# Kernel optimization log

Measured on AMD Instinct MI355X. Metric: run time of the kernel, lower is better.

## Reference

```python
import jax, jax.numpy as jnp
import numpy as np
import math
from jax import lax

B, C, T = 32, 256, 1024
KS = 64          # key_size
KERN = 3         # conv kernel size
PAD = 2          # (KERN-1)*dilation, chomped -> causal left pad
SQRT_KS = math.sqrt(KS)


def setup_inputs() -> dict:
    key = jax.random.key(0)
    ks = jax.random.split(key, 14)
    s = 0.01
    return {
        "x":  jax.random.normal(ks[0], (B, C, T), jnp.float32),
        # attention linears (stored [in, out])
        "wq": jax.random.normal(ks[1], (C, KS), jnp.float32) * s,
        "bq": jnp.zeros((KS,), jnp.float32),
        "wk": jax.random.normal(ks[2], (C, KS), jnp.float32) * s,
        "bk": jnp.zeros((KS,), jnp.float32),
        "wv": jax.random.normal(ks[3], (C, C), jnp.float32) * s,
        "bv": jnp.zeros((C,), jnp.float32),
        # weight-normed conv 1: v [out,in,k], g [out], b [out]
        "v1": jax.random.normal(ks[4], (C, C, KERN), jnp.float32) * s,
        "g1": jnp.ones((C,), jnp.float32),
        "b1": jnp.zeros((C,), jnp.float32),
        # weight-normed conv 2
        "v2": jax.random.normal(ks[5], (C, C, KERN), jnp.float32) * s,
        "g2": jnp.ones((C,), jnp.float32),
        "b2": jnp.zeros((C,), jnp.float32),
    }


def _wn_conv_relu(h, v, g, b):
    # weight_norm (dim=0): W = g * v / ||v||, norm over (in, k) per out channel
    norm = jnp.sqrt(jnp.sum(v * v, axis=(1, 2), keepdims=True))
    W = (g[:, None, None] / norm) * v
    # left-pad PAD == Conv1d(padding=PAD) + Chomp1d(PAD)  (causal conv)
    y = lax.conv_general_dilated(h, W, window_strides=(1,), padding=[(PAD, 0)],
                                 dimension_numbers=("NCH", "OIH", "NCH"))
    return jax.nn.relu(y + b[None, :, None])


def reference(x, wq, bq, wk, bk, wv, bv, v1, g1, b1, v2, g2, b2):
    t = x.shape[2]
    xt = jnp.swapaxes(x, 1, 2)                      # [B, T, C]
    q = xt @ wq + bq                                # [B, T, KS]
    k = xt @ wk + bk                                # [B, T, KS]
    v = xt @ wv + bv                                # [B, T, C]
    scores = jnp.einsum("bqd,bkd->bqk", q, k)       # [B, Tq, Tk]
    # torch mask[j][i] = 1 if i > j -> masked where key index > query index
    idx = jnp.arange(t)
    mask = idx[None, :] > idx[:, None]              # [Tq, Tk]
    scores = jnp.where(mask[None], -jnp.inf, scores)
    # NOTE: source applies softmax over dim=1 (the QUERY axis) — faithful quirk
    attn = jax.nn.softmax(scores / SQRT_KS, axis=1)  # [B, Tq, Tk]
    out_attn = jnp.einsum("bqk,bkc->bqc", attn, v)  # [B, T, C]
    out_attn = jnp.swapaxes(out_attn, 1, 2)         # [B, C, T]
    # conv stack (dropout=0 / eval)
    out = _wn_conv_relu(out_attn, v1, g1, b1)
    out = _wn_conv_relu(out, v2, g2, b2)
    # en_res branch: per-timestep scaling of x by softmaxed attention mass
    weight_x = jax.nn.softmax(jnp.sum(attn, axis=2), axis=1)  # [B, T]
    en_res_x = weight_x[:, None, :] * x                       # [B, C, T]
    # downsample is None (n_inputs == n_outputs)
    return jax.nn.relu(out + x + en_res_x)
```

## Files before the change

kernel.cpp:

```cpp
#include <hip/hip_runtime.h>
#include <math.h>

#define BB 32
#define CC 256
#define TT 1024

typedef __attribute__((ext_vector_type(4))) float f4;
typedef __attribute__((ext_vector_type(4))) float f32x4;
typedef __attribute__((ext_vector_type(16))) float f32x16;
typedef __attribute__((ext_vector_type(8))) short s8;
typedef __attribute__((ext_vector_type(4))) short s4v;

__device__ inline short f2bf(float f) {
    unsigned u = __builtin_bit_cast(unsigned, f);
    u = (u + 0x7FFFu + ((u >> 16) & 1u)) >> 16;
    return (short)u;
}

static const size_t OFF_QBF  = 0;
static const size_t OFF_KBF  = 4194304;
static const size_t OFF_VT   = 8388608;
static const size_t OFF_OA   = 25165824;
static const size_t OFF_C1   = 58720256;
static const size_t OFF_CRZ  = 75497472;
static const size_t OFF_RS   = 75628544;
static const size_t OFF_WX   = 75759616;
static const size_t OFF_W1   = 75890688;
static const size_t OFF_W2   = 76283904;
static const size_t OFF_WQKV = 76677120;

__global__ __launch_bounds__(256)
void wn_kernel(const float* __restrict__ v1, const float* __restrict__ g1,
               const float* __restrict__ v2, const float* __restrict__ g2,
               short* __restrict__ w1bf, short* __restrict__ w2bf) {
    __shared__ float red[4];
    int which = blockIdx.x >> 8, o = blockIdx.x & 255;
    const float* v = which ? v2 : v1;
    const float* g = which ? g2 : g1;
    short* wt = which ? w2bf : w1bf;
    const float* row = v + (size_t)o * 768;
    int tid = threadIdx.x, lane = tid & 63, wv_ = tid >> 6;
    float r0 = row[tid], r1 = row[tid + 256], r2 = row[tid + 512];
    float s = r0 * r0 + r1 * r1 + r2 * r2;
    for (int d = 1; d < 64; d <<= 1) s += __shfl_xor(s, d, 64);
    if (lane == 0) red[wv_] = s;
    __syncthreads();
    float scale = g[o] * rsqrtf(red[0] + red[1] + red[2] + red[3]);
    for (int j = 0; j < 3; ++j)
        wt[((size_t)(j * 256 + o)) * 256 + tid] = f2bf(scale * row[tid * 3 + j]);
}

__global__ __launch_bounds__(256)
void pack_kernel(const float* __restrict__ wq, const float* __restrict__ wk,
                 const float* __restrict__ wv, short* __restrict__ wqkvbf) {
    int n = blockIdx.x * 4 + (threadIdx.x >> 6);
    int c0 = (threadIdx.x & 63) * 4;
    for (int p = 0; p < 4; ++p) {
        int c = c0 + p;
        float w;
        if (n < 64)       w = wq[c * 64 + n];
        else if (n < 128) w = wk[c * 64 + n - 64];
        else              w = wv[c * 256 + n - 128];
        wqkvbf[(size_t)n * 256 + c] = f2bf(w);
    }
}

__global__ void transpose_kernel(const float* __restrict__ x, short* __restrict__ xt) {
    __shared__ float Tt[64 * 68];
    int tid = threadIdx.x;
    int c0 = blockIdx.x * 64, t0 = blockIdx.y * 64, b = blockIdx.z;
    for (int it = 0; it < 4; ++it) {
        int idx = tid + 256 * it;
        int cr = idx >> 4, tc = idx & 15;
        f4 v = *reinterpret_cast<const f4*>(&x[((size_t)b * CC + c0 + cr) * TT + t0 + tc * 4]);
        *reinterpret_cast<f4*>(&Tt[cr * 68 + tc * 4]) = v;
    }
    __syncthreads();
    for (int it = 0; it < 2; ++it) {
        int idx = tid + 256 * it;
        int tl = idx >> 3, seg = idx & 7;
        s8 o;
        for (int p = 0; p < 8; ++p) o[p] = f2bf(Tt[(seg * 8 + p) * 68 + tl]);
        *reinterpret_cast<s8*>(&xt[((size_t)b * TT + t0 + tl) * CC + c0 + seg * 8]) = o;
    }
}

__global__ __launch_bounds__(256, 3)
void qkv_kernel(const short* __restrict__ xt, const short* __restrict__ wqkv,
                const float* __restrict__ bq, const float* __restrict__ bk,
                const float* __restrict__ bv,
                short* __restrict__ qbf, short* __restrict__ kbf, short* __restrict__ vt) {
    __shared__ short SL[128 * 72 + 64 * 72];
    short* Asm = SL;
    short* Bsm = SL + 128 * 72;
    int tid = threadIdx.x, wv_ = tid >> 6, lane = tid & 63;
    int n15 = lane & 15, quad = lane >> 4;
    int bid = blockIdx.x;
    int r = bid & 7, n = (bid >> 3) % 6, qd = bid / 48;
    int bt = qd * 8 + r;
    int b = bt >> 3, t0 = (bt & 7) * 128;
    int n0 = n * 64;

    f32x4 acc[2][4];
    for (int i = 0; i < 2; ++i) for (int j = 0; j < 4; ++j)
        for (int p = 0; p < 4; ++p) acc[i][j][p] = 0.f;

    for (int kc = 0; kc < 4; ++kc) {
        int c0 = kc * 64;
        __syncthreads();
        for (int it = 0; it < 4; ++it) {
            int idx = tid + 256 * it;
            int row = idx >> 3, seg = idx & 7;
            *reinterpret_cast<s8*>(&Asm[row * 72 + seg * 8]) =
                *reinterpret_cast<const s8*>(&xt[((size_t)b * TT + t0 + row) * CC + c0 + seg * 8]);
        }
        for (int it = 0; it < 2; ++it) {
            int idx = tid + 256 * it;
            int row = idx >> 3, seg = idx & 7;
            *reinterpret_cast<s8*>(&Bsm[row * 72 + seg * 8]) =
                *reinterpret_cast<const s8*>(&wqkv[(size_t)(n0 + row) * 256 + c0 + seg * 8]);
        }
        __syncthreads();
        for (int ks = 0; ks < 2; ++ks)
            for (int mt2 = 0; mt2 < 2; ++mt2) {
                s8 a = *reinterpret_cast<const s8*>(&Asm[(wv_ * 32 + mt2 * 16 + n15) * 72 + quad * 8 + ks * 32]);
                for (int nt = 0; nt < 4; ++nt) {
                    s8 bb = *reinterpret_cast<const s8*>(&Bsm[(nt * 16 + n15) * 72 + quad * 8 + ks * 32]);
                    acc[mt2][nt] = __builtin_amdgcn_mfma_f32_16x16x32_bf16(a, bb, acc[mt2][nt], 0, 0, 0);
                }
            }
    }
    if (n0 < 128) {
        short* outp = (n0 == 0) ? qbf : kbf;
        const float* bias = (n0 == 0) ? bq : bk;
        for (int mt2 = 0; mt2 < 2; ++mt2)
            for (int nt = 0; nt < 4; ++nt) {
                int n_ = nt * 16 + n15;
                float bvl = bias[n_];
                for (int reg = 0; reg < 4; ++reg) {
                    int t = t0 + wv_ * 32 + mt2 * 16 + quad * 4 + reg;
                    outp[((size_t)b * TT + t) * 64 + n_] = f2bf(acc[mt2][nt][reg] + bvl);
                }
            }
    } else {
        int cbase = n0 - 128;
        __syncthreads();
        short* Tw = SL + wv_ * 3072;
        for (int mt2 = 0; mt2 < 2; ++mt2)
            for (int nt = 0; nt < 4; ++nt) {
                int n_ = nt * 16 + n15;
                float bvl = bv[cbase + n_];
                for (int reg = 0; reg < 4; ++reg)
                    Tw[n_ * 48 + mt2 * 16 + quad * 4 + reg] = f2bf(acc[mt2][nt][reg] + bvl);
            }
        for (int p = 0; p < 4; ++p) {
            int n_ = (lane >> 2) + 16 * p;
            int seg = lane & 3;
            s8 vv = *reinterpret_cast<const s8*>(&Tw[n_ * 48 + seg * 8]);
            *reinterpret_cast<s8*>(&vt[((size_t)b * CC + cbase + n_) * TT + t0 + wv_ * 32 + seg * 8]) = vv;
        }
    }
}

__global__ __launch_bounds__(512, 2)
void colz_kernel(const short* __restrict__ qbf, const short* __restrict__ kbf,
                 float* __restrict__ colrz) {
    __shared__ short Qs[4][64 * 72];
    __shared__ short Ks[64 * 72];
    __shared__ float redz[8][2][32];
    int tid = threadIdx.x, wv_ = tid >> 6, lane = tid & 63;
    int l31 = lane & 31, lh = lane >> 5;
    int qh = wv_ & 1, ti = wv_ >> 1;
    int b = blockIdx.x & 31, pr = blockIdx.x >> 5;
    int kts[2] = {pr, 15 - pr};
    int row = tid >> 3, sg = (tid & 7) * 8;

    s8 kr = *reinterpret_cast<const s8*>(&kbf[((size_t)b * TT + kts[0] * 64 + row) * 64 + sg]);
    s8 qreg[4];
    for (int j = 0; j < 4; ++j) {
        int t = kts[0] + j; if (t > 15) t = 15;
        qreg[j] = *reinterpret_cast<const s8*>(&qbf[((size_t)b * TT + t * 64 + row) * 64 + sg]);
    }

    for (int ph = 0; ph < 2; ++ph) {
        int kt = kts[ph];
        float zl[2] = {0.f, 0.f};
        for (int u = kt; u < 16; u += 4) {
            __syncthreads();
            if (u == kt) *reinterpret_cast<s8*>(&Ks[row * 72 + sg]) = kr;
            for (int j = 0; j < 4; ++j)
                *reinterpret_cast<s8*>(&Qs[j][row * 72 + sg]) = qreg[j];
            __syncthreads();
            int nu = u + 4;
            if (nu < 16) {
                for (int j = 0; j < 4; ++j) {
                    int t = nu + j; if (t > 15) t = 15;
                    qreg[j] = *reinterpret_cast<const s8*>(&qbf[((size_t)b * TT + t * 64 + row) * 64 + sg]);
                }
            } else if (ph == 0) {
                int k2 = kts[1];
                kr = *reinterpret_cast<const s8*>(&kbf[((size_t)b * TT + k2 * 64 + row) * 64 + sg]);
                for (int j = 0; j < 4; ++j) {
                    int t = k2 + j; if (t > 15) t = 15;
                    qreg[j] = *reinterpret_cast<const s8*>(&qbf[((size_t)b * TT + t * 64 + row) * 64 + sg]);
                }
            }
            int qtw = u + ti;
            if (qtw < 16) {
                for (int kh = 0; kh < 2; ++kh) {
                    f32x16 s;
                    for (int p = 0; p < 16; ++p) s[p] = 0.f;
                    for (int kc = 0; kc < 4; ++kc) {
                        s8 a  = *reinterpret_cast<const s8*>(&Qs[ti][(qh * 32 + l31) * 72 + kc * 16 + lh * 8]);
                        s8 bb = *reinterpret_cast<const s8*>(&Ks[(kh * 32 + l31) * 72 + kc * 16 + lh * 8]);
                        s = __builtin_amdgcn_mfma_f32_32x32x16_bf16(a, bb, s, 0, 0, 0);
                    }
                    int kg = kt * 64 + kh * 32 + l31;
                    int qb0 = qtw * 64 + qh * 32 + 4 * lh;
                    if (qtw > kt) {
                        for (int reg = 0; reg < 16; ++reg)
                            zl[kh] += __expf(s[reg] * 0.125f);
                    } else {
                        for (int reg = 0; reg < 16; ++reg) {
                            int rr = (reg & 3) + 8 * (reg >> 2);
                            if (qb0 + rr >= kg) zl[kh] += __expf(s[reg] * 0.125f);
                        }
                    }
                }
            }
        }
        for (int kh = 0; kh < 2; ++kh) {
            float zc = zl[kh] + __shfl_xor(zl[kh], 32, 64);
            if (lane < 32) redz[wv_][kh][lane] = zc;
        }
        __syncthreads();
        if (tid < 64) {
            int kh = tid >> 5, kk = tid & 31;
            float Z = 0.f;
            for (int w = 0; w < 8; ++w) Z += redz[w][kh][kk];
            colrz[(size_t)b * TT + kt * 64 + tid] = 1.0f / Z;
        }
        __syncthreads();
    }
}

__global__ __launch_bounds__(512, 2)
void attn_kernel(const short* __restrict__ qbf, const short* __restrict__ kbf,
                 const short* __restrict__ vt, const float* __restrict__ colrz,
                 short* __restrict__ oab, float* __restrict__ rowsum) {
    __shared__ short Ks[2][64 * 72];
    __shared__ short Ps[2][64 * 72];
    __shared__ short Vs[2][256 * 72];
    __shared__ float redR[4][64];
    int tid = threadIdx.x, wv_ = tid >> 6, lane = tid & 63;
    int l31 = lane & 31, lh = lane >> 5;
    int wq2 = wv_ & 1;
    int wk4 = wv_ >> 1;
    int ksub = wk4 >> 1;
    int kh2 = wk4 & 1;
    int wcq = wv_ >> 1;
    int b = blockIdx.x & 31, pr = blockIdx.x >> 5;
    int qts[2] = {15 - pr, pr};
    int row = tid >> 3, sg = (tid & 7) * 8;

    s8 kreg[2], vreg[2][4];
    for (int j = 0; j < 2; ++j) {
        kreg[j] = *reinterpret_cast<const s8*>(&kbf[((size_t)b * TT + j * 64 + row) * 64 + sg]);
        for (int it = 0; it < 4; ++it) {
            int idx = tid + 512 * it;
            int vr = idx >> 3, seg = idx & 7;
            vreg[j][it] = *reinterpret_cast<const s8*>(&vt[((size_t)b * CC + vr) * TT + j * 64 + seg * 8]);
        }
    }

    for (int ph = 0; ph < 2; ++ph) {
        int qt = qts[ph];
        s8 qf[4];
        for (int kc = 0; kc < 4; ++kc)
            qf[kc] = *reinterpret_cast<const s8*>(
                &qbf[((size_t)b * TT + qt * 64 + wq2 * 32 + l31) * 64 + kc * 16 + lh * 8]);
        f32x16 acc[2];
        for (int i = 0; i < 2; ++i) for (int p = 0; p < 16; ++p) acc[i][p] = 0.f;
        float rsum[16];
        for (int i = 0; i < 16; ++i) rsum[i] = 0.f;

        for (int kt = 0; kt <= qt; kt += 2) {
            bool two = (kt + 1 <= qt);
            __syncthreads();
            *reinterpret_cast<s8*>(&Ks[0][row * 72 + sg]) = kreg[0];
            if (two) *reinterpret_cast<s8*>(&Ks[1][row * 72 + sg]) = kreg[1];
            for (int it = 0; it < 4; ++it) {
                int idx = tid + 512 * it;
                int vr = idx >> 3, seg = idx & 7;
                *reinterpret_cast<s8*>(&Vs[0][vr * 72 + seg * 8]) = vreg[0][it];
                if (two) *reinterpret_cast<s8*>(&Vs[1][vr * 72 + seg * 8]) = vreg[1][it];
            }
            __syncthreads();
            int nkt = (kt + 2 <= qt) ? kt + 2 : ((ph == 0) ? 0 : -1);
            if (nkt >= 0) {
                for (int j = 0; j < 2; ++j) {
                    kreg[j] = *reinterpret_cast<const s8*>(&kbf[((size_t)b * TT + (nkt + j) * 64 + row) * 64 + sg]);
                    for (int it = 0; it < 4; ++it) {
                        int idx = tid + 512 * it;
                        int vr = idx >> 3, seg = idx & 7;
                        vreg[j][it] = *reinterpret_cast<const s8*>(&vt[((size_t)b * CC + vr) * TT + (nkt + j) * 64 + seg * 8]);
                    }
                }
            }
            int mykt = kt + ksub;
            if (two || ksub == 0) {
                f32x16 s;
                for (int p = 0; p < 16; ++p) s[p] = 0.f;
                for (int kc = 0; kc < 4; ++kc) {
                    s8 bb = *reinterpret_cast<const s8*>(&Ks[ksub][(kh2 * 32 + l31) * 72 + kc * 16 + lh * 8]);
                    s = __builtin_amdgcn_mfma_f32_32x32x16_bf16(qf[kc], bb, s, 0, 0, 0);
                }
                int kg = mykt * 64 + kh2 * 32 + l31;
                float rz = colrz[(size_t)b * TT + kg];
                bool full = (mykt < qt);
                int qb0 = qt * 64 + wq2 * 32 + 4 * lh;
                for (int reg = 0; reg < 16; ++reg) {
                    int rr = (reg & 3) + 8 * (reg >> 2);
                    float p = 0.f;
                    if (full || qb0 + rr >= kg) p = __expf(s[reg] * 0.125f) * rz;
                    rsum[reg] += p;
                    Ps[ksub][(wq2 * 32 + rr + 4 * lh) * 72 + kh2 * 32 + l31] = f2bf(p);
                }
            }
            __syncthreads();
            int jmax = two ? 2 : 1;
            for (int j = 0; j < jmax; ++j)
                for (int kc = 0; kc < 4; ++kc) {
                    s8 a = *reinterpret_cast<const s8*>(&Ps[j][(wq2 * 32 + l31) * 72 + kc * 16 + lh * 8]);
                    for (int nt = 0; nt < 2; ++nt) {
                        s8 bb = *reinterpret_cast<const s8*>(&Vs[j][(wcq * 64 + nt * 32 + l31) * 72 + kc * 16 + lh * 8]);
                        acc[nt] = __builtin_amdgcn_mfma_f32_32x32x16_bf16(a, bb, acc[nt], 0, 0, 0);
                    }
                }
        }
        for (int reg = 0; reg < 16; ++reg) {
            float v = rsum[reg];
            v += __shfl_xor(v, 1, 64);
            v += __shfl_xor(v, 2, 64);
            v += __shfl_xor(v, 4, 64);
            v += __shfl_xor(v, 8, 64);
            v += __shfl_xor(v, 16, 64);
            int rr = (reg & 3) + 8 * (reg >> 2);
            if (l31 == 0) redR[wk4][wq2 * 32 + rr + 4 * lh] = v;
        }
        for (int nt = 0; nt < 2; ++nt) {
            int c = wcq * 64 + nt * 32 + l31;
            for (int reg = 0; reg < 16; ++reg) {
                int q = qt * 64 + wq2 * 32 + (reg & 3) + 8 * (reg >> 2) + 4 * lh;
                oab[((size_t)b * TT + q) * CC + c] = f2bf(acc[nt][reg]);
            }
        }
        __syncthreads();
        if (tid < 64)
            rowsum[(size_t)b * TT + qt * 64 + tid] =
                redR[0][tid] + redR[1][tid] + redR[2][tid] + redR[3][tid];
        __syncthreads();
    }
}

__global__ __launch_bounds__(256, 3)
void conv_kernel(const void* __restrict__ inp, int in_is_fp32,
                 const short* __restrict__ wbf, const float* __restrict__ bias,
                 void* __restrict__ outp, int out_is_bf16,
                 const float* __restrict__ xres, const float* __restrict__ wxv,
                 int fuse_final) {
    __shared__ short SL[130 * 72 + 3 * 64 * 72];
    short* As = SL;
    short* Bs = SL + 130 * 72;
    int tid = threadIdx.x, wv_ = tid >> 6, lane = tid & 63;
    int n15 = lane & 15, quad = lane >> 4;
    int bid = blockIdx.x;
    int r = bid & 7;
    int n0 = ((bid >> 3) & 3) << 6;
    int bm = (bid >> 5) * 8 + r;
    int b = bm >> 3, mt = bm & 7;
    int t0 = mt * 128;
    f32x4 acc[2][4];
    for (int i = 0; i < 2; ++i) for (int j = 0; j < 4; ++j)
        for (int p = 0; p < 4; ++p) acc[i][j][p] = 0.f;

    for (int kc = 0; kc < 4; ++kc) {
        int c0 = kc * 64;
        __syncthreads();
        if (in_is_fp32) {
            const float* in = (const float*)inp;
            for (int it = 0; it < 9; ++it) {
                int idx = tid + 256 * it;
                int row = idx >> 4, fc = idx & 15;
                if (row < 130) {
                    int t = t0 + row - 2;
                    s4v st;
                    if (t >= 0) {
                        f4 v = *reinterpret_cast<const f4*>(&in[((size_t)b * TT + t) * CC + c0 + fc * 4]);
                        for (int p = 0; p < 4; ++p) st[p] = f2bf(v[p]);
                    } else { for (int p = 0; p < 4; ++p) st[p] = 0; }
                    *reinterpret_cast<s4v*>(&As[row * 72 + fc * 4]) = st;
                }
            }
        } else {
            const short* in = (const short*)inp;
            for (int it = 0; it < 5; ++it) {
                int idx = tid + 256 * it;
                int row = idx >> 3, seg = idx & 7;
                if (row < 130) {
                    int t = t0 + row - 2;
                    s8 st;
                    if (t >= 0) st = *reinterpret_cast<const s8*>(&in[((size_t)b * TT + t) * CC + c0 + seg * 8]);
                    else for (int p = 0; p < 8; ++p) st[p] = 0;
                    *reinterpret_cast<s8*>(&As[row * 72 + seg * 8]) = st;
                }
            }
        }
        for (int it = 0; it < 6; ++it) {
            int idx = tid + 256 * it;
            int row = idx >> 3, seg = idx & 7;
            int j = row >> 6, o = row & 63;
            *reinterpret_cast<s8*>(&Bs[row * 72 + seg * 8]) =
                *reinterpret_cast<const s8*>(&wbf[((size_t)(j * 256 + n0 + o)) * 256 + c0 + seg * 8]);
        }
        __syncthreads();
        for (int j = 0; j < 3; ++j)
            for (int ks = 0; ks < 2; ++ks)
                for (int mt2 = 0; mt2 < 2; ++mt2) {
                    s8 a = *reinterpret_cast<const s8*>(&As[(wv_ * 32 + mt2 * 16 + n15 + j) * 72 + quad * 8 + ks * 32]);
                    for (int nt = 0; nt < 4; ++nt) {
                        s8 bb = *reinterpret_cast<const s8*>(&Bs[(j * 64 + nt * 16 + n15) * 72 + quad * 8 + ks * 32]);
                        acc[mt2][nt] = __builtin_amdgcn_mfma_f32_16x16x32_bf16(a, bb, acc[mt2][nt], 0, 0, 0);
                    }
                }
    }
    if (!fuse_final) {
        for (int mt2 = 0; mt2 < 2; ++mt2)
            for (int nt = 0; nt < 4; ++nt) {
                int o = n0 + nt * 16 + n15;
                float bvl = bias[o];
                for (int reg = 0; reg < 4; ++reg) {
                    int t = t0 + wv_ * 32 + mt2 * 16 + quad * 4 + reg;
                    float v = fmaxf(acc[mt2][nt][reg] + bvl, 0.f);
                    if (out_is_bf16) ((short*)outp)[((size_t)b * TT + t) * CC + o] = f2bf(v);
                    else             ((float*)outp)[((size_t)b * TT + t) * CC + o] = v;
                }
            }
    } else {
        float* Ft = (float*)SL;
        __syncthreads();
        for (int mt2 = 0; mt2 < 2; ++mt2)
            for (int nt = 0; nt < 4; ++nt) {
                int ol = nt * 16 + n15;
                float bvl = bias[n0 + ol];
                for (int reg = 0; reg < 4; ++reg) {
                    int tl = wv_ * 32 + mt2 * 16 + quad * 4 + reg;
                    Ft[tl * 67 + ol] = fmaxf(acc[mt2][nt][reg] + bvl, 0.f);
                }
            }
        __syncthreads();
        int c_l = tid >> 5;
        int t_l = (tid & 31) * 4;
        f4 wv4 = *reinterpret_cast<const f4*>(&wxv[(size_t)b * TT + t0 + t_l]);
        for (int pass = 0; pass < 8; ++pass) {
            int c = n0 + pass * 8 + c_l;
            f4 xv = *reinterpret_cast<const f4*>(&xres[((size_t)b * CC + c) * TT + t0 + t_l]);
            f4 rr;
            for (int p = 0; p < 4; ++p)
                rr[p] = fmaxf(Ft[(t_l + p) * 67 + pass * 8 + c_l] + xv[p] * (1.f + wv4[p]), 0.f);
            *reinterpret_cast<f4*>(&((float*)outp)[((size_t)b * CC + c) * TT + t0 + t_l]) = rr;
        }
    }
}

__global__ void rowsm_kernel(const float* __restrict__ rowsum, float* __restrict__ wx) {
    __shared__ float red[256];
    int b = blockIdx.x, tid = threadIdx.x;
    float v[4];
    float m = -1e30f;
    for (int r = 0; r < 4; ++r) { v[r] = rowsum[(size_t)b * TT + tid + 256 * r]; m = fmaxf(m, v[r]); }
    red[tid] = m; __syncthreads();
    for (int s = 128; s > 0; s >>= 1) { if (tid < s) red[tid] = fmaxf(red[tid], red[tid + s]); __syncthreads(); }
    m = red[0]; __syncthreads();
    float e[4], zs = 0.f;
    for (int r = 0; r < 4; ++r) { e[r] = __expf(v[r] - m); zs += e[r]; }
    red[tid] = zs; __syncthreads();
    for (int s = 128; s > 0; s >>= 1) { if (tid < s) red[tid] += red[tid + s]; __syncthreads(); }
    float rz = 1.0f / red[0];
    for (int r = 0; r < 4; ++r) wx[(size_t)b * TT + tid + 256 * r] = e[r] * rz;
}

extern "C" void kernel_launch(void* const* d_in, const int* in_sizes, int n_in,
                              void* d_out, int out_size, void* d_ws, size_t ws_size,
                              hipStream_t stream) {
    (void)in_sizes; (void)n_in; (void)out_size; (void)ws_size;
    const float* x  = (const float*)d_in[0];
    const float* wq = (const float*)d_in[1];
    const float* bq = (const float*)d_in[2];
    const float* wk = (const float*)d_in[3];
    const float* bk = (const float*)d_in[4];
    const float* wv = (const float*)d_in[5];
    const float* bv = (const float*)d_in[6];
    const float* v1 = (const float*)d_in[7];
    const float* g1 = (const float*)d_in[8];
    const float* b1 = (const float*)d_in[9];
    const float* v2 = (const float*)d_in[10];
    const float* g2 = (const float*)d_in[11];
    const float* b2 = (const float*)d_in[12];
    char* ws = (char*)d_ws;
    float* out = (float*)d_out;

    short* qbf  = (short*)(ws + OFF_QBF);
    short* kbf  = (short*)(ws + OFF_KBF);
    short* vt   = (short*)(ws + OFF_VT);
    short* xt   = (short*)(ws + OFF_OA);
    short* oab  = (short*)(ws + OFF_OA);
    short* c1   = (short*)(ws + OFF_C1);
    float* crz  = (float*)(ws + OFF_CRZ);
    float* rs   = (float*)(ws + OFF_RS);
    float* wxb  = (float*)(ws + OFF_WX);
    short* w1bf = (short*)(ws + OFF_W1);
    short* w2bf = (short*)(ws + OFF_W2);
    short* wqkv = (short*)(ws + OFF_WQKV);

    wn_kernel<<<dim3(512), dim3(256), 0, stream>>>(v1, g1, v2, g2, w1bf, w2bf);
    pack_kernel<<<dim3(96), dim3(256), 0, stream>>>(wq, wk, wv, wqkv);
    transpose_kernel<<<dim3(4, 16, 32), dim3(256), 0, stream>>>(x, xt);
    qkv_kernel<<<dim3(1536), dim3(256), 0, stream>>>(xt, wqkv, bq, bk, bv, qbf, kbf, vt);
    colz_kernel<<<dim3(256), dim3(512), 0, stream>>>(qbf, kbf, crz);
    attn_kernel<<<dim3(256), dim3(512), 0, stream>>>(qbf, kbf, vt, crz, oab, rs);
    rowsm_kernel<<<dim3(32), dim3(256), 0, stream>>>(rs, wxb);
    conv_kernel<<<dim3(1024), dim3(256), 0, stream>>>(oab, 0, w1bf, b1, c1, 1,
                                                      nullptr, nullptr, 0);
    conv_kernel<<<dim3(1024), dim3(256), 0, stream>>>(c1, 0, w2bf, b2, out, 0,
                                                      x, wxb, 1);
}
```

Baseline: 225.8 us.

## Warp-specialize attention kernel into QK/softmax producers and PV consumers

Splits the attention block into 1024 threads. Eight producer waves compute QK^T scores and exp-weighted P tiles, while eight consumer waves run the P·V MFMAs on the previous tile, with K/V/P double-buffered in shared memory. Q is staged in LDS rather than held in registers. The goal is to overlap the softmax/score stage with the PV matmul and shorten the serial chain per key tile. The cost is two barriers per single key tile instead of per pair, and heavier register and LDS pressure at 1024 threads under launch_bounds(1024,4).

```diff
diff --git a/kernel.cpp b/kernel.cpp
--- a/kernel.cpp
+++ b/kernel.cpp
@@ -244,122 +244,146 @@
     }
 }
 
-__global__ __launch_bounds__(512, 2)
+__global__ __launch_bounds__(1024, 4)
 void attn_kernel(const short* __restrict__ qbf, const short* __restrict__ kbf,
                  const short* __restrict__ vt, const float* __restrict__ colrz,
                  short* __restrict__ oab, float* __restrict__ rowsum) {
+    __shared__ short Qs[64 * 72];
     __shared__ short Ks[2][64 * 72];
     __shared__ short Ps[2][64 * 72];
     __shared__ short Vs[2][256 * 72];
-    __shared__ float redR[4][64];
+    __shared__ float redR[2][64];
     int tid = threadIdx.x, wv_ = tid >> 6, lane = tid & 63;
     int l31 = lane & 31, lh = lane >> 5;
-    int wq2 = wv_ & 1;
-    int wk4 = wv_ >> 1;
-    int ksub = wk4 >> 1;
-    int kh2 = wk4 & 1;
-    int wcq = wv_ >> 1;
+    bool prod = (wv_ < 8);
+    int pw = wv_ & 7;
+    int wq2 = pw & 1, wk2 = (pw >> 1) & 1, w4 = pw >> 2;
+    int wcq = pw >> 1;
     int b = blockIdx.x & 31, pr = blockIdx.x >> 5;
     int qts[2] = {15 - pr, pr};
-    int row = tid >> 3, sg = (tid & 7) * 8;
-
-    s8 kreg[2], vreg[2][4];
-    for (int j = 0; j < 2; ++j) {
-        kreg[j] = *reinterpret_cast<const s8*>(&kbf[((size_t)b * TT + j * 64 + row) * 64 + sg]);
-        for (int it = 0; it < 4; ++it) {
-            int idx = tid + 512 * it;
-            int vr = idx >> 3, seg = idx & 7;
-            vreg[j][it] = *reinterpret_cast<const s8*>(&vt[((size_t)b * CC + vr) * TT + j * 64 + seg * 8]);
-        }
-    }
+    int ctid = tid & 511;
+    int row = ctid >> 3, sg = (ctid & 7) * 8;
 
     for (int ph = 0; ph < 2; ++ph) {
         int qt = qts[ph];
-        s8 qf[4];
-        for (int kc = 0; kc < 4; ++kc)
-            qf[kc] = *reinterpret_cast<const s8*>(
-                &qbf[((size_t)b * TT + qt * 64 + wq2 * 32 + l31) * 64 + kc * 16 + lh * 8]);
+        __syncthreads();
         f32x16 acc[2];
-        for (int i = 0; i < 2; ++i) for (int p = 0; p < 16; ++p) acc[i][p] = 0.f;
-        float rsum[16];
-        for (int i = 0; i < 16; ++i) rsum[i] = 0.f;
-
-        for (int kt = 0; kt <= qt; kt += 2) {
-            bool two = (kt + 1 <= qt);
-            __syncthreads();
-            *reinterpret_cast<s8*>(&Ks[0][row * 72 + sg]) = kreg[0];
-            if (two) *reinterpret_cast<s8*>(&Ks[1][row * 72 + sg]) = kreg[1];
+        float rsum[8];
+        s8 kreg, vreg[4];
+        if (prod) {
+            for (int i = 0; i < 8; ++i) rsum[i] = 0.f;
+            s8 qr0 = *reinterpret_cast<const s8*>(&qbf[((size_t)b * TT + qt * 64 + row) * 64 + sg]);
+            kreg = *reinterpret_cast<const s8*>(&kbf[((size_t)b * TT + row) * 64 + sg]);
+            *reinterpret_cast<s8*>(&Qs[row * 72 + sg]) = qr0;
+            *reinterpret_cast<s8*>(&Ks[0][row * 72 + sg]) = kreg;
+            if (qt >= 1)
+                kreg = *reinterpret_cast<const s8*>(&kbf[((size_t)b * TT + 64 + row) * 64 + sg]);
+        } else {
+            for (int i = 0; i < 2; ++i) for (int p = 0; p < 16; ++p) acc[i][p] = 0.f;
             for (int it = 0; it < 4; ++it) {
-                int idx = tid + 512 * it;
+                int idx = ctid + 512 * it;
                 int vr = idx >> 3, seg = idx & 7;
-                *reinterpret_cast<s8*>(&Vs[0][vr * 72 + seg * 8]) = vreg[0][it];
-                if (two) *reinterpret_cast<s8*>(&Vs[1][vr * 72 + seg * 8]) = vreg[1][it];
-            }
-            __syncthreads();
-            int nkt = (kt + 2 <= qt) ? kt + 2 : ((ph == 0) ? 0 : -1);
-            if (nkt >= 0) {
-                for (int j = 0; j < 2; ++j) {
-                    kreg[j] = *reinterpret_cast<const s8*>(&kbf[((size_t)b * TT + (nkt + j) * 64 + row) * 64 + sg]);
-                    for (int it = 0; it < 4; ++it) {
-                        int idx = tid + 512 * it;
-                        int vr = idx >> 3, seg = idx & 7;
-                        vreg[j][it] = *reinterpret_cast<const s8*>(&vt[((size_t)b * CC + vr) * TT + (nkt + j) * 64 + seg * 8]);
-                    }
-                }
-            }
-            int mykt = kt + ksub;
-            if (two || ksub == 0) {
+                vreg[it] = *reinterpret_cast<const s8*>(&vt[((size_t)b * CC + vr) * TT + seg * 8]);
+                *reinterpret_cast<s8*>(&Vs[0][vr * 72 + seg * 8]) = vreg[it];
+            }
+            if (qt >= 1)
+                for (int it = 0; it < 4; ++it) {
+                    int idx = ctid + 512 * it;
+                    int vr = idx >> 3, seg = idx & 7;
+                    vreg[it] = *reinterpret_cast<const s8*>(&vt[((size_t)b * CC + vr) * TT + 64 + seg * 8]);
+                }
+        }
+        __syncthreads();
+        int cb = 0;
+        for (int kt = 0; kt <= qt; ++kt) {
+            if (prod) {
                 f32x16 s;
                 for (int p = 0; p < 16; ++p) s[p] = 0.f;
                 for (int kc = 0; kc < 4; ++kc) {
-                    s8 bb = *reinterpret_cast<const s8*>(&Ks[ksub][(kh2 * 32 + l31) * 72 + kc * 16 + lh * 8]);
-                    s = __builtin_amdgcn_mfma_f32_32x32x16_bf16(qf[kc], bb, s, 0, 0, 0);
-                }
-                int kg = mykt * 64 + kh2 * 32 + l31;
+                    s8 a  = *reinterpret_cast<const s8*>(&Qs[(wq2 * 32 + l31) * 72 + kc * 16 + lh * 8]);
+                    s8 bb = *reinterpret_cast<const s8*>(&Ks[cb][(wk2 * 32 + l31) * 72 + kc * 16 + lh * 8]);
+                    s = __builtin_amdgcn_mfma_f32_32x32x16_bf16(a, bb, s, 0, 0, 0);
+                }
+                int kg = kt * 64 + wk2 * 32 + l31;
                 float rz = colrz[(size_t)b * TT + kg];
-                bool full = (mykt < qt);
+                bool full = (kt < qt);
                 int qb0 = qt * 64 + wq2 * 32 + 4 * lh;
-                for (int reg = 0; reg < 16; ++reg) {
+                for (int r = 0; r < 8; ++r) {
+                    int reg = w4 * 8 + r;
                     int rr = (reg & 3) + 8 * (reg >> 2);
                     float p = 0.f;
                     if (full || qb0 + rr >= kg) p = __expf(s[reg] * 0.125f) * rz;
-                    rsum[reg] += p;
-                    Ps[ksub][(wq2 * 32 + rr + 4 * lh) * 72 + kh2 * 32 + l31] = f2bf(p);
-                }
-            }
-            __syncthreads();
-            int jmax = two ? 2 : 1;
-            for (int j = 0; j < jmax; ++j)
+                    rsum[r] += p;
+                    Ps[cb][(wq2 * 32 + rr + 4 * lh) * 72 + wk2 * 32 + l31] = f2bf(p);
+                }
+            } else if (kt > 0) {
+                const short* Pr = Ps[cb ^ 1];
+                const short* Vr = Vs[cb ^ 1];
                 for (int kc = 0; kc < 4; ++kc) {
-                    s8 a = *reinterpret_cast<const s8*>(&Ps[j][(wq2 * 32 + l31) * 72 + kc * 16 + lh * 8]);
+                    s8 a = *reinterpret_cast<const s8*>(&Pr[(wq2 * 32 + l31) * 72 + kc * 16 + lh * 8]);
                     for (int nt = 0; nt < 2; ++nt) {
-                        s8 bb = *reinterpret_cast<const s8*>(&Vs[j][(wcq * 64 + nt * 32 + l31) * 72 + kc * 16 + lh * 8]);
+                        s8 bb = *reinterpret_cast<const s8*>(&Vr[(wcq * 64 + nt * 32 + l31) * 72 + kc * 16 + lh * 8]);
                         acc[nt] = __builtin_amdgcn_mfma_f32_32x32x16_bf16(a, bb, acc[nt], 0, 0, 0);
                     }
                 }
-        }
-        for (int reg = 0; reg < 16; ++reg) {
-            float v = rsum[reg];
-            v += __shfl_xor(v, 1, 64);
-            v += __shfl_xor(v, 2, 64);
-            v += __shfl_xor(v, 4, 64);
-            v += __shfl_xor(v, 8, 64);
-            v += __shfl_xor(v, 16, 64);
-            int rr = (reg & 3) + 8 * (reg >> 2);
-            if (l31 == 0) redR[wk4][wq2 * 32 + rr + 4 * lh] = v;
-        }
-        for (int nt = 0; nt < 2; ++nt) {
-            int c = wcq * 64 + nt * 32 + l31;
-            for (int reg = 0; reg < 16; ++reg) {
-                int q = qt * 64 + wq2 * 32 + (reg & 3) + 8 * (reg >> 2) + 4 * lh;
-                oab[((size_t)b * TT + q) * CC + c] = f2bf(acc[nt][reg]);
-            }
-        }
-        __syncthreads();
-        if (tid < 64)
-            rowsum[(size_t)b * TT + qt * 64 + tid] =
-                redR[0][tid] + redR[1][tid] + redR[2][tid] + redR[3][tid];
-        __syncthreads();
+            }
+            __syncthreads();
+            if (kt < qt) {
+                if (prod) {
+                    *reinterpret_cast<s8*>(&Ks[cb ^ 1][row * 72 + sg]) = kreg;
+                    if (kt + 2 <= qt)
+                        kreg = *reinterpret_cast<const s8*>(&kbf[((size_t)b * TT + (kt + 2) * 64 + row) * 64 + sg]);
+                } else {
+                    for (int it = 0; it < 4; ++it) {
+                        int idx = ctid + 512 * it;
+                        int vr = idx >> 3, seg = idx & 7;
+                        *reinterpret_cast<s8*>(&Vs[cb ^ 1][vr * 72 + seg * 8]) = vreg[it];
+                    }
+                    if (kt + 2 <= qt)
+                        for (int it = 0; it < 4; ++it) {
+                            int idx = ctid + 512 * it;
+                            int vr = idx >> 3, seg = idx & 7;
+                            vreg[it] = *reinterpret_cast<const s8*>(&vt[((size_t)b * CC + vr) * TT + (kt + 2) * 64 + seg * 8]);
+                        }
+                }
+            }
+            __syncthreads();
+            cb ^= 1;
+        }
+        if (!prod) {
+            const short* Pr = Ps[cb ^ 1];
+            const short* Vr = Vs[cb ^ 1];
+            for (int kc = 0; kc < 4; ++kc) {
+                s8 a = *reinterpret_cast<const s8*>(&Pr[(wq2 * 32 + l31) * 72 + kc * 16 + lh * 8]);
+                for (int nt = 0; nt < 2; ++nt) {
+                    s8 bb = *reinterpret_cast<const s8*>(&Vr[(wcq * 64 + nt * 32 + l31) * 72 + kc * 16 + lh * 8]);
+                    acc[nt] = __builtin_amdgcn_mfma_f32_32x32x16_bf16(a, bb, acc[nt], 0, 0, 0);
+                }
+            }
+        } else {
+            for (int r = 0; r < 8; ++r) {
+                float v = rsum[r];
+                v += __shfl_xor(v, 1, 64);
+                v += __shfl_xor(v, 2, 64);
+                v += __shfl_xor(v, 4, 64);
+                v += __shfl_xor(v, 8, 64);
+                v += __shfl_xor(v, 16, 64);
+                int reg = w4 * 8 + r;
+                int rr = (reg & 3) + 8 * (reg >> 2);
+                if (l31 == 0) redR[wk2][wq2 * 32 + rr + 4 * lh] = v;
+            }
+        }
+        __syncthreads();
+        if (tid < 64) rowsum[(size_t)b * TT + qt * 64 + tid] = redR[0][tid] + redR[1][tid];
+        if (!prod) {
+            for (int nt = 0; nt < 2; ++nt) {
+                int c = wcq * 64 + nt * 32 + l31;
+                for (int reg = 0; reg < 16; ++reg) {
+                    int q = qt * 64 + wq2 * 32 + (reg & 3) + 8 * (reg >> 2) + 4 * lh;
+                    oab[((size_t)b * TT + q) * CC + c] = f2bf(acc[nt][reg]);
+                }
+            }
+        }
     }
 }
 
@@ -528,7 +552,7 @@
     transpose_kernel<<<dim3(4, 16, 32), dim3(256), 0, stream>>>(x, xt);
     qkv_kernel<<<dim3(1536), dim3(256), 0, stream>>>(xt, wqkv, bq, bk, bv, qbf, kbf, vt);
     colz_kernel<<<dim3(256), dim3(512), 0, stream>>>(qbf, kbf, crz);
-    attn_kernel<<<dim3(256), dim3(512), 0, stream>>>(qbf, kbf, vt, crz, oab, rs);
+    attn_kernel<<<dim3(256), dim3(1024), 0, stream>>>(qbf, kbf, vt, crz, oab, rs);
     rowsm_kernel<<<dim3(32), dim3(256), 0, stream>>>(rs, wxb);
     conv_kernel<<<dim3(1024), dim3(256), 0, stream>>>(oab, 0, w1bf, b1, c1, 1,
                                                       nullptr, nullptr, 0);
```

After: 280.5 us. +24.2%, slower.

## Split attention query tiles in half to double block count

Applied to the files above, without the earlier changes.

The attention kernel now gives each block 32 query rows instead of 64, launches 512 blocks instead of 256, and processes one key tile per iteration instead of two. Each wave computes a 32x32 score tile and its share of the exp/P writes, and each wave owns 32 output channels. Shared memory drops and launch bounds allow 4 blocks per CU, aiming for more parallelism and occupancy on the 256-CU device. In exchange each key tile and the V tiles are loaded twice as often overall, the score MFMA is duplicated across wave pairs, and there are more barriers per unit of work.

```diff
diff --git a/kernel.cpp b/kernel.cpp
--- a/kernel.cpp
+++ b/kernel.cpp
@@ -244,121 +244,109 @@
     }
 }
 
-__global__ __launch_bounds__(512, 2)
+__global__ __launch_bounds__(512, 4)
 void attn_kernel(const short* __restrict__ qbf, const short* __restrict__ kbf,
                  const short* __restrict__ vt, const float* __restrict__ colrz,
                  short* __restrict__ oab, float* __restrict__ rowsum) {
-    __shared__ short Ks[2][64 * 72];
-    __shared__ short Ps[2][64 * 72];
-    __shared__ short Vs[2][256 * 72];
-    __shared__ float redR[4][64];
+    __shared__ short Qs[32 * 72];
+    __shared__ short Ks[64 * 72];
+    __shared__ short Ps[32 * 72];
+    __shared__ short Vs[256 * 72];
+    __shared__ float redR[2][32];
     int tid = threadIdx.x, wv_ = tid >> 6, lane = tid & 63;
     int l31 = lane & 31, lh = lane >> 5;
-    int wq2 = wv_ & 1;
-    int wk4 = wv_ >> 1;
-    int ksub = wk4 >> 1;
-    int kh2 = wk4 & 1;
-    int wcq = wv_ >> 1;
-    int b = blockIdx.x & 31, pr = blockIdx.x >> 5;
+    int wk2 = wv_ & 1, wdup = wv_ >> 1;
+    int bid = blockIdx.x;
+    int b = bid & 31, pr = (bid >> 5) & 7, qh = bid >> 8;
     int qts[2] = {15 - pr, pr};
     int row = tid >> 3, sg = (tid & 7) * 8;
 
-    s8 kreg[2], vreg[2][4];
-    for (int j = 0; j < 2; ++j) {
-        kreg[j] = *reinterpret_cast<const s8*>(&kbf[((size_t)b * TT + j * 64 + row) * 64 + sg]);
+    s8 kreg, vreg[4];
+    {
+        kreg = *reinterpret_cast<const s8*>(&kbf[((size_t)b * TT + row) * 64 + sg]);
         for (int it = 0; it < 4; ++it) {
             int idx = tid + 512 * it;
             int vr = idx >> 3, seg = idx & 7;
-            vreg[j][it] = *reinterpret_cast<const s8*>(&vt[((size_t)b * CC + vr) * TT + j * 64 + seg * 8]);
+            vreg[it] = *reinterpret_cast<const s8*>(&vt[((size_t)b * CC + vr) * TT + seg * 8]);
         }
     }
 
     for (int ph = 0; ph < 2; ++ph) {
         int qt = qts[ph];
-        s8 qf[4];
-        for (int kc = 0; kc < 4; ++kc)
-            qf[kc] = *reinterpret_cast<const s8*>(
-                &qbf[((size_t)b * TT + qt * 64 + wq2 * 32 + l31) * 64 + kc * 16 + lh * 8]);
-        f32x16 acc[2];
-        for (int i = 0; i < 2; ++i) for (int p = 0; p < 16; ++p) acc[i][p] = 0.f;
-        float rsum[16];
-        for (int i = 0; i < 16; ++i) rsum[i] = 0.f;
-
-        for (int kt = 0; kt <= qt; kt += 2) {
-            bool two = (kt + 1 <= qt);
+        s8 qr0;
+        if (tid < 256)
+            qr0 = *reinterpret_cast<const s8*>(
+                &qbf[((size_t)b * TT + qt * 64 + qh * 32 + row) * 64 + sg]);
+        f32x16 acc;
+        for (int p = 0; p < 16; ++p) acc[p] = 0.f;
+        float rsum[4] = {0.f, 0.f, 0.f, 0.f};
+
+        for (int kt = 0; kt <= qt; ++kt) {
             __syncthreads();
-            *reinterpret_cast<s8*>(&Ks[0][row * 72 + sg]) = kreg[0];
-            if (two) *reinterpret_cast<s8*>(&Ks[1][row * 72 + sg]) = kreg[1];
+            if (kt == 0 && tid < 256) *reinterpret_cast<s8*>(&Qs[row * 72 + sg]) = qr0;
+            *reinterpret_cast<s8*>(&Ks[row * 72 + sg]) = kreg;
             for (int it = 0; it < 4; ++it) {
                 int idx = tid + 512 * it;
                 int vr = idx >> 3, seg = idx & 7;
-                *reinterpret_cast<s8*>(&Vs[0][vr * 72 + seg * 8]) = vreg[0][it];
-                if (two) *reinterpret_cast<s8*>(&Vs[1][vr * 72 + seg * 8]) = vreg[1][it];
+                *reinterpret_cast<s8*>(&Vs[vr * 72 + seg * 8]) = vreg[it];
             }
             __syncthreads();
-            int nkt = (kt + 2 <= qt) ? kt + 2 : ((ph == 0) ? 0 : -1);
+            int nkt = (kt < qt) ? kt + 1 : ((ph == 0) ? 0 : -1);
             if (nkt >= 0) {
-                for (int j = 0; j < 2; ++j) {
-                    kreg[j] = *reinterpret_cast<const s8*>(&kbf[((size_t)b * TT + (nkt + j) * 64 + row) * 64 + sg]);
-                    for (int it = 0; it < 4; ++it) {
-                        int idx = tid + 512 * it;
-                        int vr = idx >> 3, seg = idx & 7;
-                        vreg[j][it] = *reinterpret_cast<const s8*>(&vt[((size_t)b * CC + vr) * TT + (nkt + j) * 64 + seg * 8]);
-                    }
-                }
-            }
-            int mykt = kt + ksub;
-            if (two || ksub == 0) {
-                f32x16 s;
-                for (int p = 0; p < 16; ++p) s[p] = 0.f;
-                for (int kc = 0; kc < 4; ++kc) {
-                    s8 bb = *reinterpret_cast<const s8*>(&Ks[ksub][(kh2 * 32 + l31) * 72 + kc * 16 + lh * 8]);
-                    s = __builtin_amdgcn_mfma_f32_32x32x16_bf16(qf[kc], bb, s, 0, 0, 0);
-                }
-                int kg = mykt * 64 + kh2 * 32 + l31;
-                float rz = colrz[(size_t)b * TT + kg];
-                bool full = (mykt < qt);
-                int qb0 = qt * 64 + wq2 * 32 + 4 * lh;
-                for (int reg = 0; reg < 16; ++reg) {
-                    int rr = (reg & 3) + 8 * (reg >> 2);
-                    float p = 0.f;
-                    if (full || qb0 + rr >= kg) p = __expf(s[reg] * 0.125f) * rz;
-                    rsum[reg] += p;
-                    Ps[ksub][(wq2 * 32 + rr + 4 * lh) * 72 + kh2 * 32 + l31] = f2bf(p);
-                }
+                kreg = *reinterpret_cast<const s8*>(&kbf[((size_t)b * TT + nkt * 64 + row) * 64 + sg]);
+                for (int it = 0; it < 4; ++it) {
+                    int idx = tid + 512 * it;
+                    int vr = idx >> 3, seg = idx & 7;
+                    vreg[it] = *reinterpret_cast<const s8*>(&vt[((size_t)b * CC + vr) * TT + nkt * 64 + seg * 8]);
+                }
+            }
+            f32x16 s;
+            for (int p = 0; p < 16; ++p) s[p] = 0.f;
+            for (int kc = 0; kc < 4; ++kc) {
+                s8 a  = *reinterpret_cast<const s8*>(&Qs[l31 * 72 + kc * 16 + lh * 8]);
+                s8 bb = *reinterpret_cast<const s8*>(&Ks[(wk2 * 32 + l31) * 72 + kc * 16 + lh * 8]);
+                s = __builtin_amdgcn_mfma_f32_32x32x16_bf16(a, bb, s, 0, 0, 0);
+            }
+            int kg = kt * 64 + wk2 * 32 + l31;
+            float rz = colrz[(size_t)b * TT + kg];
+            bool full = (kt < qt);
+            int qb0 = qt * 64 + qh * 32 + 4 * lh;
+            for (int r = 0; r < 4; ++r) {
+                int reg = wdup * 4 + r;
+                int rr = (reg & 3) + 8 * (reg >> 2);
+                float p = 0.f;
+                if (full || qb0 + rr >= kg) p = __expf(s[reg] * 0.125f) * rz;
+                rsum[r] += p;
+                Ps[(rr + 4 * lh) * 72 + wk2 * 32 + l31] = f2bf(p);
             }
             __syncthreads();
-            int jmax = two ? 2 : 1;
-            for (int j = 0; j < jmax; ++j)
-                for (int kc = 0; kc < 4; ++kc) {
-                    s8 a = *reinterpret_cast<const s8*>(&Ps[j][(wq2 * 32 + l31) * 72 + kc * 16 + lh * 8]);
-                    for (int nt = 0; nt < 2; ++nt) {
-                        s8 bb = *reinterpret_cast<const s8*>(&Vs[j][(wcq * 64 + nt * 32 + l31) * 72 + kc * 16 + lh * 8]);
-                        acc[nt] = __builtin_amdgcn_mfma_f32_32x32x16_bf16(a, bb, acc[nt], 0, 0, 0);
-                    }
-                }
-        }
-        for (int reg = 0; reg < 16; ++reg) {
-            float v = rsum[reg];
+            for (int kc = 0; kc < 4; ++kc) {
+                s8 a  = *reinterpret_cast<const s8*>(&Ps[l31 * 72 + kc * 16 + lh * 8]);
+                s8 bb = *reinterpret_cast<const s8*>(&Vs[(wv_ * 32 + l31) * 72 + kc * 16 + lh * 8]);
+                acc = __builtin_amdgcn_mfma_f32_32x32x16_bf16(a, bb, acc, 0, 0, 0);
+            }
+        }
+        for (int r = 0; r < 4; ++r) {
+            float v = rsum[r];
             v += __shfl_xor(v, 1, 64);
             v += __shfl_xor(v, 2, 64);
             v += __shfl_xor(v, 4, 64);
             v += __shfl_xor(v, 8, 64);
             v += __shfl_xor(v, 16, 64);
+            int reg = wdup * 4 + r;
             int rr = (reg & 3) + 8 * (reg >> 2);
-            if (l31 == 0) redR[wk4][wq2 * 32 + rr + 4 * lh] = v;
-        }
-        for (int nt = 0; nt < 2; ++nt) {
-            int c = wcq * 64 + nt * 32 + l31;
+            if (l31 == 0) redR[wk2][rr + 4 * lh] = v;
+        }
+        {
+            int c = wv_ * 32 + l31;
             for (int reg = 0; reg < 16; ++reg) {
-                int q = qt * 64 + wq2 * 32 + (reg & 3) + 8 * (reg >> 2) + 4 * lh;
-                oab[((size_t)b * TT + q) * CC + c] = f2bf(acc[nt][reg]);
-            }
-        }
-        __syncthreads();
-        if (tid < 64)
-            rowsum[(size_t)b * TT + qt * 64 + tid] =
-                redR[0][tid] + redR[1][tid] + redR[2][tid] + redR[3][tid];
+                int q = qt * 64 + qh * 32 + (reg & 3) + 8 * (reg >> 2) + 4 * lh;
+                oab[((size_t)b * TT + q) * CC + c] = f2bf(acc[reg]);
+            }
+        }
+        __syncthreads();
+        if (tid < 32)
+            rowsum[(size_t)b * TT + qt * 64 + qh * 32 + tid] = redR[0][tid] + redR[1][tid];
         __syncthreads();
     }
 }
@@ -528,7 +516,7 @@
     transpose_kernel<<<dim3(4, 16, 32), dim3(256), 0, stream>>>(x, xt);
     qkv_kernel<<<dim3(1536), dim3(256), 0, stream>>>(xt, wqkv, bq, bk, bv, qbf, kbf, vt);
     colz_kernel<<<dim3(256), dim3(512), 0, stream>>>(qbf, kbf, crz);
-    attn_kernel<<<dim3(256), dim3(512), 0, stream>>>(qbf, kbf, vt, crz, oab, rs);
+    attn_kernel<<<dim3(512), dim3(512), 0, stream>>>(qbf, kbf, vt, crz, oab, rs);
     rowsm_kernel<<<dim3(32), dim3(256), 0, stream>>>(rs, wxb);
     conv_kernel<<<dim3(1024), dim3(256), 0, stream>>>(oab, 0, w1bf, b1, c1, 1,
                                                       nullptr, nullptr, 0);
```

Result: slower. 235.4 us (+4.3%).
